# Performance work log

Hardware: AMD Instinct MI355X
Metric: run time of the kernel (lower is better)

The kernel has to match this reference:

```python
import jax, jax.numpy as jnp
import numpy as np

LAM = 0.001  # init kwarg lam; agg='mean'


def setup_inputs() -> dict:
    key = jax.random.key(0)
    k1, k2 = jax.random.split(key)
    B, C, N = 4, 2, 8192
    inputs = jax.random.normal(k1, (B, C, N), dtype=jnp.float32)
    coords = jax.random.normal(k2, (B, N, 3), dtype=jnp.float32)
    return {"inputs": inputs, "coords": coords}


def _pairwise_dist(c):
    # c: (B, N, 3) -> (B, N, N) Euclidean distances (cdist p=2)
    sq = jnp.sum(c * c, axis=-1)                      # (B, N)
    d2 = sq[:, :, None] + sq[:, None, :] - 2.0 * jnp.einsum('bnd,bmd->bnm', c, c)
    return jnp.sqrt(jnp.maximum(d2, 0.0))


def reference(inputs, coords):
    coords = coords[:, :, :3]
    d = _pairwise_dist(coords)                        # (B, N, N)
    w = jax.nn.softmax(inputs, axis=1)[:, 1, :]       # (B, N) foreground prob
    dpp = d * w[:, :, None] * w[:, None, :]
    return jnp.mean(dpp) * LAM
```

## Files before the change

kernel.cpp:

```cpp
#include <hip/hip_runtime.h>

#define NFULL 8192
#define BATCH 4
#define TT 256
#define NT (NFULL / TT)
#define JOBS_PER_B (NT * (NT + 1) / 2)
#define TOTAL_JOBS (BATCH * JOBS_PER_B)
#define IR 4
#define LAMBDA 0.001

__device__ __forceinline__ void load_point(const float* __restrict__ coords,
                                           const float* __restrict__ inputs,
                                           int b, int n,
                                           float& x, float& y, float& z,
                                           float& sq, float& w) {
    const float* cp = coords + (size_t)(b * NFULL + n) * 3;
    x = cp[0]; y = cp[1]; z = cp[2];
    sq = fmaf(x, x, fmaf(y, y, z * z));
    float a0 = inputs[(size_t)b * 2 * NFULL + n];
    float a1 = inputs[(size_t)b * 2 * NFULL + NFULL + n];
    w = 1.0f / (1.0f + __expf(a0 - a1));
}

__global__ void KUNi_zero_ws(double* ws) { ws[0] = 0.0; }

__global__ void KUNi_finalize(const double* __restrict__ ws, float* __restrict__ out) {
    const double scale = LAMBDA / ((double)BATCH * (double)NFULL * (double)NFULL);
    out[0] = (float)(ws[0] * scale);
}

__global__ __launch_bounds__(64)
void KUNi_dpp_kernel(const float* __restrict__ inputs,
                     const float* __restrict__ coords,
                     double* __restrict__ acc_out) {
    __shared__ float sX[TT], sY[TT], sZ[TT], sSQ[TT], sW[TT];

    const int tid = threadIdx.x;
    int bid = blockIdx.x;
    const int b = bid / JOBS_PER_B;
    int p = bid - b * JOBS_PER_B;

    int ti = 0;
    while (p >= NT - ti) { p -= NT - ti; ++ti; }
    const int tj = ti + p;

    for (int jl = tid; jl < TT; jl += 64) {
        float x, y, z, sq, w;
        load_point(coords, inputs, b, tj * TT + jl, x, y, z, sq, w);
        sX[jl] = -2.0f * x;
        sY[jl] = -2.0f * y;
        sZ[jl] = -2.0f * z;
        sSQ[jl] = sq;
        sW[jl]  = w;
    }

    float ix[IR], iy[IR], iz[IR], isq[IR], iw[IR], acc[IR];
#pragma unroll
    for (int k = 0; k < IR; ++k) {
        load_point(coords, inputs, b, ti * TT + tid + k * 64,
                   ix[k], iy[k], iz[k], isq[k], iw[k]);
        acc[k] = 0.0f;
    }

    __syncthreads();

#pragma unroll 2
    for (int jj = 0; jj < TT; ++jj) {
        const float jx = sX[jj];
        const float jy = sY[jj];
        const float jz = sZ[jj];
        const float jsq = sSQ[jj];
        const float jw = sW[jj];
#pragma unroll
        for (int k = 0; k < IR; ++k) {
            float t = isq[k] + jsq;
            t = fmaf(jx, ix[k], t);
            t = fmaf(jy, iy[k], t);
            t = fmaf(jz, iz[k], t);
            t = fmaxf(t, 0.0f);
            float s = __builtin_amdgcn_sqrtf(t);
            acc[k] = fmaf(s, jw, acc[k]);
        }
    }

    float v = 0.0f;
#pragma unroll
    for (int k = 0; k < IR; ++k) v = fmaf(iw[k], acc[k], v);
    if (ti != tj) v *= 2.0f;

#pragma unroll
    for (int off = 32; off > 0; off >>= 1) v += __shfl_xor(v, off, 64);
    if (tid == 0) atomicAdd(acc_out, (double)v);
}

extern "C" void kernel_launch(void* const* d_in, const int* in_sizes, int n_in,
                              void* d_out, int out_size, void* d_ws, size_t ws_size,
                              hipStream_t stream) {
    const float* inputs = (const float*)d_in[0];
    const float* coords = (const float*)d_in[1];
    float* out = (float*)d_out;
    double* acc = (double*)d_ws;

    KUNi_zero_ws<<<1, 1, 0, stream>>>(acc);
    KUNi_dpp_kernel<<<TOTAL_JOBS, 64, 0, stream>>>(inputs, coords, acc);
    KUNi_finalize<<<1, 1, 0, stream>>>(acc, out);
}
```

Baseline: 103.6 us.

## Split j-tile across four waves per block and replace atomics with per-block partials

```diff
diff --git a/kernel.cpp b/kernel.cpp
--- a/kernel.cpp
+++ b/kernel.cpp
@@ -7,7 +7,10 @@
 #define JOBS_PER_B (NT * (NT + 1) / 2)
 #define TOTAL_JOBS (BATCH * JOBS_PER_B)
 #define IR 4
+#define JW 64
 #define LAMBDA 0.001
+
+struct alignas(16) F4 { float x, y, z, sq; };
 
 __device__ __forceinline__ void load_point(const float* __restrict__ coords,
                                            const float* __restrict__ inputs,
@@ -22,20 +25,34 @@
     w = 1.0f / (1.0f + __expf(a0 - a1));
 }
 
-__global__ void KUNi_zero_ws(double* ws) { ws[0] = 0.0; }
-
-__global__ void KUNi_finalize(const double* __restrict__ ws, float* __restrict__ out) {
-    const double scale = LAMBDA / ((double)BATCH * (double)NFULL * (double)NFULL);
-    out[0] = (float)(ws[0] * scale);
+__global__ void KUNi_finalize(const float* __restrict__ partials,
+                              float* __restrict__ out) {
+    const int tid = threadIdx.x;
+    const int lane = tid & 63, wv = tid >> 6;
+    double s = 0.0;
+    for (int i = tid; i < TOTAL_JOBS; i += 256) s += (double)partials[i];
+#pragma unroll
+    for (int off = 32; off > 0; off >>= 1) s += __shfl_xor(s, off, 64);
+    __shared__ double sd[4];
+    if (lane == 0) sd[wv] = s;
+    __syncthreads();
+    if (tid == 0) {
+        const double scale = LAMBDA / ((double)BATCH * (double)NFULL * (double)NFULL);
+        out[0] = (float)((sd[0] + sd[1] + sd[2] + sd[3]) * scale);
+    }
 }
 
-__global__ __launch_bounds__(64)
+__global__ __launch_bounds__(256)
 void KUNi_dpp_kernel(const float* __restrict__ inputs,
                      const float* __restrict__ coords,
-                     double* __restrict__ acc_out) {
-    __shared__ float sX[TT], sY[TT], sZ[TT], sSQ[TT], sW[TT];
+                     float* __restrict__ partials) {
+    __shared__ F4 sj[TT];
+    __shared__ float sw[TT];
+    __shared__ float sred[4];
 
     const int tid = threadIdx.x;
+    const int lane = tid & 63;
+    const int wv = tid >> 6;
     int bid = blockIdx.x;
     const int b = bid / JOBS_PER_B;
     int p = bid - b * JOBS_PER_B;
@@ -44,39 +61,37 @@
     while (p >= NT - ti) { p -= NT - ti; ++ti; }
     const int tj = ti + p;
 
-    for (int jl = tid; jl < TT; jl += 64) {
+    {
         float x, y, z, sq, w;
-        load_point(coords, inputs, b, tj * TT + jl, x, y, z, sq, w);
-        sX[jl] = -2.0f * x;
-        sY[jl] = -2.0f * y;
-        sZ[jl] = -2.0f * z;
-        sSQ[jl] = sq;
-        sW[jl]  = w;
+        load_point(coords, inputs, b, tj * TT + tid, x, y, z, sq, w);
+        sj[tid].x = -2.0f * x;
+        sj[tid].y = -2.0f * y;
+        sj[tid].z = -2.0f * z;
+        sj[tid].sq = sq;
+        sw[tid] = w;
     }
 
     float ix[IR], iy[IR], iz[IR], isq[IR], iw[IR], acc[IR];
 #pragma unroll
     for (int k = 0; k < IR; ++k) {
-        load_point(coords, inputs, b, ti * TT + tid + k * 64,
+        load_point(coords, inputs, b, ti * TT + lane + k * 64,
                    ix[k], iy[k], iz[k], isq[k], iw[k]);
         acc[k] = 0.0f;
     }
 
     __syncthreads();
 
-#pragma unroll 2
-    for (int jj = 0; jj < TT; ++jj) {
-        const float jx = sX[jj];
-        const float jy = sY[jj];
-        const float jz = sZ[jj];
-        const float jsq = sSQ[jj];
-        const float jw = sW[jj];
+    const int j0 = wv * JW;
+#pragma unroll 4
+    for (int jj = j0; jj < j0 + JW; ++jj) {
+        const F4 jv = sj[jj];
+        const float jw = sw[jj];
 #pragma unroll
         for (int k = 0; k < IR; ++k) {
-            float t = isq[k] + jsq;
-            t = fmaf(jx, ix[k], t);
-            t = fmaf(jy, iy[k], t);
-            t = fmaf(jz, iz[k], t);
+            float t = isq[k] + jv.sq;
+            t = fmaf(jv.x, ix[k], t);
+            t = fmaf(jv.y, iy[k], t);
+            t = fmaf(jv.z, iz[k], t);
             t = fmaxf(t, 0.0f);
             float s = __builtin_amdgcn_sqrtf(t);
             acc[k] = fmaf(s, jw, acc[k]);
@@ -90,7 +105,9 @@
 
 #pragma unroll
     for (int off = 32; off > 0; off >>= 1) v += __shfl_xor(v, off, 64);
-    if (tid == 0) atomicAdd(acc_out, (double)v);
+    if (lane == 0) sred[wv] = v;
+    __syncthreads();
+    if (tid == 0) partials[bid] = sred[0] + sred[1] + sred[2] + sred[3];
 }
 
 extern "C" void kernel_launch(void* const* d_in, const int* in_sizes, int n_in,
@@ -99,9 +116,8 @@
     const float* inputs = (const float*)d_in[0];
     const float* coords = (const float*)d_in[1];
     float* out = (float*)d_out;
-    double* acc = (double*)d_ws;
+    float* partials = (float*)d_ws;
 
-    KUNi_zero_ws<<<1, 1, 0, stream>>>(acc);
-    KUNi_dpp_kernel<<<TOTAL_JOBS, 64, 0, stream>>>(inputs, coords, acc);
-    KUNi_finalize<<<1, 1, 0, stream>>>(acc, out);
+    KUNi_dpp_kernel<<<TOTAL_JOBS, 256, 0, stream>>>(inputs, coords, partials);
+    KUNi_finalize<<<1, 256, 0, stream>>>(partials, out);
 }
```

Result: faster. 88.13 us (-14.9%).
